# Optimization experiments

Hardware: AMD Instinct MI355X
Metric: run time of the kernel (lower is better)

The kernel has to match this reference:

```python
import jax, jax.numpy as jnp
import numpy as np

CAPACITY_FACTOR = 1.2


def setup_inputs() -> dict:
    key = jax.random.key(0)
    k1, k2 = jax.random.split(key, 2)
    D, E = 1024, 64
    x = jax.random.normal(k1, (8, 4096, D), dtype=jnp.float32)
    # xavier-uniform-ish router weight, zero bias (as in __init__)
    limit = np.sqrt(6.0 / (D + E)).astype(np.float32)
    W = jax.random.uniform(k2, (E, D), dtype=jnp.float32, minval=-limit, maxval=limit)
    b = jnp.zeros((E,), dtype=jnp.float32)
    return {"x": x, "W": W, "b": b, "detach_inputs": 0}


def reference(x, W, b, detach_inputs):
    bsz, seqlen, D = x.shape
    E = W.shape[0]                      # num experts == max_steps
    N = bsz * seqlen                    # num tokens
    x_flat = x.reshape(N, D)
    if detach_inputs:
        x_flat = jax.lax.stop_gradient(x_flat)
    logits = x_flat @ W.T + b           # [N, E]

    # expert-choice capacity (static python ints)
    k = max(1, int(N / max(1, E) * CAPACITY_FACTOR))
    k = min(k, N)

    # per-expert top-k over tokens: [E, k]
    topk_vals, topk_idx = jax.lax.top_k(logits.T, k)
    cand_tok = topk_idx.reshape(-1)                       # [E*k] token ids
    cand_exp = jnp.repeat(jnp.arange(E, dtype=jnp.int32), k)  # [E*k]
    cand_val = topk_vals.reshape(-1)                      # [E*k]

    # scatter-amax: best candidate logit per token (torch scatter_reduce_ 'amax')
    best_val = jnp.full((N,), -jnp.inf, dtype=logits.dtype).at[cand_tok].max(cand_val)

    # candidates that achieve the per-token max; dedup -> one expert per token
    # (tie-break: smallest expert index, matching first-occurrence after sort)
    eq = cand_val == best_val[cand_tok]
    exp_cand = jnp.where(eq, cand_exp, E).astype(jnp.int32)
    token_exp = jnp.full((N,), E, dtype=jnp.int32).at[cand_tok].min(exp_cand)
    selected = token_exp < E                              # token was picked by some expert
    assigned_expert = jnp.where(selected, token_exp, -1)  # [N], -1 = unassigned

    # load-balance loss from per-expert counts (bincount of assigned experts)
    sel_f = selected.astype(logits.dtype)
    counts = jnp.zeros((E,), dtype=logits.dtype).at[jnp.where(selected, token_exp, 0)].add(sel_f)
    mean_load = counts.mean()
    load_balance_loss = ((counts - mean_load) ** 2).mean() / (mean_load + 1e-9)

    best_val_out = jnp.where(selected, best_val, jnp.zeros((), logits.dtype))
    return (best_val_out, assigned_expert, selected, load_balance_loss)
```

## Files before the change

kernel.cpp:

```cpp
#include <hip/hip_runtime.h>
#include <math.h>

typedef __attribute__((ext_vector_type(4))) double d4;

__device__ inline unsigned fkey(float f) {
  unsigned bits = __float_as_uint(f);
  return (bits & 0x80000000u) ? ~bits : (bits | 0x80000000u);
}

__global__ __launch_bounds__(512, 4) void logits_fused_kernel(
    const float* __restrict__ x, const float* __restrict__ W,
    const float* __restrict__ bias, float* __restrict__ logits,
    float* __restrict__ logitsT, int N, int D) {
  __shared__ __attribute__((aligned(16))) double xs64[64 * 66];
  __shared__ __attribute__((aligned(16))) double ws64[64 * 66];
  __shared__ unsigned s_fl;

  const int tid = threadIdx.x;
  const int tok0 = blockIdx.x * 64;
  const int l = tid & 63;
  const int l15 = l & 15;
  const int lk = l >> 4;

  double* pA = ws64;
  double* pB = ws64 + 64;
  if (tid < 64) {
    pA[l15 * 4 + lk] = (double)(l15 * 4 + lk + 1);
    pB[lk * 16 + l15] = (double)(l15 * 7 + lk * 3 + 2);
  }
  __syncthreads();
  if (tid < 64) {
    double a = pA[l15 * 4 + lk];
    double b = pB[lk * 16 + l15];
    d4 pacc = (d4)0.0;
    pacc = __builtin_amdgcn_mfma_f64_16x16x4f64(a, b, pacc, 0, 0, 0);
    unsigned res = 4;
    for (int m = 3; m >= 0; --m) {
      bool ok = true;
#pragma unroll
      for (int i = 0; i < 4; ++i) {
        int tr_ = (m < 2) ? ((m == 0) ? 4 * lk + i : lk + 4 * i) : l15;
        int tc_ = (m < 2) ? l15 : ((m == 2) ? 4 * lk + i : lk + 4 * i);
        double ref = 0.0;
#pragma unroll
        for (int kk = 0; kk < 4; ++kk) ref += pA[tr_ * 4 + kk] * pB[kk * 16 + tc_];
        ok = ok && (pacc[i] == ref);
      }
      if (__all(ok)) res = (unsigned)m;
    }
    if (l == 0) s_fl = res;
  }
  __syncthreads();
  const unsigned fl = s_fl;
  __syncthreads();

  if (fl < 4u) {
    const int w = tid >> 6;
    const int rb = (w & 3) * 16;
    const int cb = (w >> 2) * 32;

    d4 acc[2];
    acc[0] = (d4)0.0;
    acc[1] = (d4)0.0;

    const int r0 = tid >> 4;
    const int c40 = tid & 15;

    float4 rx0, rx1, rw0, rw1;
    rx0 = *(const float4*)(x + (size_t)(tok0 + r0) * D + c40 * 4);
    rx1 = *(const float4*)(x + (size_t)(tok0 + 32 + r0) * D + c40 * 4);
    rw0 = *(const float4*)(W + (size_t)r0 * D + c40 * 4);
    rw1 = *(const float4*)(W + (size_t)(32 + r0) * D + c40 * 4);

    const int nch = D >> 6;
    const int xa0 = (rb + l15) * 66 + lk;
    const int ba0 = (cb + l15) * 66 + lk;

    for (int c = 0; c < nch; ++c) {
      {
        double* d0 = xs64 + r0 * 66 + c40 * 4;
        *(double2*)(d0) = make_double2((double)rx0.x, (double)rx0.y);
        *(double2*)(d0 + 2) = make_double2((double)rx0.z, (double)rx0.w);
        double* d1 = xs64 + (32 + r0) * 66 + c40 * 4;
        *(double2*)(d1) = make_double2((double)rx1.x, (double)rx1.y);
        *(double2*)(d1 + 2) = make_double2((double)rx1.z, (double)rx1.w);
        double* e0 = ws64 + r0 * 66 + c40 * 4;
        *(double2*)(e0) = make_double2((double)rw0.x, (double)rw0.y);
        *(double2*)(e0 + 2) = make_double2((double)rw0.z, (double)rw0.w);
        double* e1 = ws64 + (32 + r0) * 66 + c40 * 4;
        *(double2*)(e1) = make_double2((double)rw1.x, (double)rw1.y);
        *(double2*)(e1 + 2) = make_double2((double)rw1.z, (double)rw1.w);
      }
      __syncthreads();
      if (c + 1 < nch) {
        int kc = (c + 1) << 6;
        rx0 = *(const float4*)(x + (size_t)(tok0 + r0) * D + kc + c40 * 4);
        rx1 = *(const float4*)(x + (size_t)(tok0 + 32 + r0) * D + kc + c40 * 4);
        rw0 = *(const float4*)(W + (size_t)r0 * D + kc + c40 * 4);
        rw1 = *(const float4*)(W + (size_t)(32 + r0) * D + kc + c40 * 4);
      }
#pragma unroll
      for (int s = 0; s < 16; ++s) {
        double a = xs64[xa0 + 4 * s];
        double b0 = ws64[ba0 + 4 * s];
        double b1 = ws64[ba0 + 16 * 66 + 4 * s];
        acc[0] = __builtin_amdgcn_mfma_f64_16x16x4f64(a, b0, acc[0], 0, 0, 0);
        acc[1] = __builtin_amdgcn_mfma_f64_16x16x4f64(a, b1, acc[1], 0, 0, 0);
      }
      __syncthreads();
    }

    float* ls = (float*)xs64;
#pragma unroll
    for (int ct = 0; ct < 2; ++ct) {
#pragma unroll
      for (int i = 0; i < 4; ++i) {
        int tr_, tc_;
        if (fl < 2u) { tc_ = l15; tr_ = (fl == 0u) ? 4 * lk + i : lk + 4 * i; }
        else         { tr_ = l15; tc_ = (fl == 2u) ? 4 * lk + i : lk + 4 * i; }
        int col = cb + ct * 16 + tc_;
        ls[(rb + tr_) * 68 + col] = (float)(acc[ct][i] + (double)bias[col]);
      }
    }
    __syncthreads();
#pragma unroll
    for (int it = 0; it < 2; ++it) {
      int slot = it * 512 + tid;
      int row = slot >> 4, c4 = slot & 15;
      float4 v = {ls[row * 68 + c4 * 4 + 0], ls[row * 68 + c4 * 4 + 1],
                  ls[row * 68 + c4 * 4 + 2], ls[row * 68 + c4 * 4 + 3]};
      *(float4*)(logits + (size_t)(tok0 + row) * 64 + c4 * 4) = v;
    }
#pragma unroll
    for (int it = 0; it < 2; ++it) {
      int slot = it * 512 + tid;
      int e = slot >> 4, t4 = slot & 15;
      float4 v = {ls[(t4 * 4 + 0) * 68 + e], ls[(t4 * 4 + 1) * 68 + e],
                  ls[(t4 * 4 + 2) * 68 + e], ls[(t4 * 4 + 3) * 68 + e]};
      *(float4*)(logitsT + (size_t)e * N + tok0 + t4 * 4) = v;
    }
  } else {
    for (int o = tid; o < 64 * 64; o += 512) {
      int row = o >> 6, col = o & 63;
      const float* xp = x + (size_t)(tok0 + row) * D;
      const float* wp = W + (size_t)col * D;
      double s = 0.0;
      for (int kk = 0; kk < D; ++kk)
        s = fma((double)xp[kk], (double)wp[kk], s);
      float v = (float)(s + (double)bias[col]);
      logits[(size_t)(tok0 + row) * 64 + col] = v;
      logitsT[(size_t)col * N + tok0 + row] = v;
    }
  }
}

template <int KPT4>
__global__ __launch_bounds__(1024) void select_kernel(
    const float* __restrict__ logitsT, unsigned* __restrict__ ukeys,
    int N, int k) {
  __shared__ unsigned long long part[16];
  __shared__ unsigned s_cur;
  const int e = blockIdx.x;
  const int tid = threadIdx.x;
  const int wid = tid >> 6;
  const int lane = tid & 63;

  const float4* src = (const float4*)(logitsT + (size_t)e * N);
  unsigned key[KPT4 > 0 ? KPT4 * 4 : 4];
  if (KPT4 > 0) {
#pragma unroll
    for (int i = 0; i < (KPT4 > 0 ? KPT4 : 1); ++i) {
      float4 v = src[tid + i * 1024];
      key[i * 4 + 0] = fkey(v.x);
      key[i * 4 + 1] = fkey(v.y);
      key[i * 4 + 2] = fkey(v.z);
      key[i * 4 + 3] = fkey(v.w);
    }
  }

  unsigned cur = 0;
  for (int s = 30; s >= 0; s -= 2) {
    unsigned c1 = cur | (1u << s);
    unsigned c2 = cur | (2u << s);
    unsigned c3 = cur | (3u << s);
    unsigned n1 = 0, n2 = 0, n3 = 0;
    if (KPT4 > 0) {
#pragma unroll
      for (int i = 0; i < (KPT4 > 0 ? KPT4 * 4 : 1); ++i) {
        unsigned u = key[i];
        n1 += (u >= c1) ? 1u : 0u;
        n2 += (u >= c2) ? 1u : 0u;
        n3 += (u >= c3) ? 1u : 0u;
      }
    } else {
      for (int i = tid; i < (N >> 2); i += 1024) {
        float4 v = src[i];
        unsigned u0 = fkey(v.x), u1 = fkey(v.y), u2 = fkey(v.z), u3 = fkey(v.w);
        n1 += (u0 >= c1) + (u1 >= c1) + (u2 >= c1) + (u3 >= c1);
        n2 += (u0 >= c2) + (u1 >= c2) + (u2 >= c2) + (u3 >= c2);
        n3 += (u0 >= c3) + (u1 >= c3) + (u2 >= c3) + (u3 >= c3);
      }
    }
    unsigned long long pk = (unsigned long long)n1 |
                            ((unsigned long long)n2 << 21) |
                            ((unsigned long long)n3 << 42);
#pragma unroll
    for (int off = 32; off; off >>= 1) pk += __shfl_xor(pk, off);
    if (lane == 0) part[wid] = pk;
    __syncthreads();
    if (tid == 0) {
      unsigned long long t = 0;
#pragma unroll
      for (int w = 0; w < 16; ++w) t += part[w];
      unsigned m1 = (unsigned)(t & 0x1FFFFFu);
      unsigned m2 = (unsigned)((t >> 21) & 0x1FFFFFu);
      unsigned m3 = (unsigned)(t >> 42);
      unsigned kk = (unsigned)k;
      unsigned nxt = cur;
      if (m3 >= kk) nxt = c3;
      else if (m2 >= kk) nxt = c2;
      else if (m1 >= kk) nxt = c1;
      s_cur = nxt;
    }
    __syncthreads();
    cur = s_cur;
  }
  if (tid == 0) ukeys[e] = cur;
}

__global__ __launch_bounds__(256) void assign_kernel(
    const float* __restrict__ logits, const unsigned* __restrict__ ukeys,
    float* __restrict__ out, int N) {
  const int lane = threadIdx.x & 63;
  const int token = blockIdx.x * 4 + (threadIdx.x >> 6);

  float v = logits[(size_t)token * 64 + lane];
  unsigned u = fkey(v);
  bool cand = (u >= ukeys[lane]);
  float cv = cand ? v : -INFINITY;
  float m = cv;
#pragma unroll
  for (int off = 32; off; off >>= 1) m = fmaxf(m, __shfl_xor(m, off));
  unsigned long long mask = __ballot(cand && (v == m));
  bool sel = (mask != 0ull);
  int minexp = sel ? (__ffsll((long long)mask) - 1) : -1;

  if (lane == 0) {
    out[token] = sel ? m : 0.0f;
    out[N + token] = (float)minexp;
    out[2 * N + token] = sel ? 1.0f : 0.0f;
  }
}

__global__ __launch_bounds__(1024) void count_loss_kernel(
    const float* __restrict__ assigned, float* __restrict__ out, int N) {
  __shared__ unsigned hist[16][64];
  const int tid = threadIdx.x;
  const int wid = tid >> 6;
  hist[wid][tid & 63] = 0u;
  __syncthreads();
  const float4* src = (const float4*)assigned;
  for (int i = tid; i < (N >> 2); i += 1024) {
    float4 v = src[i];
    int e0 = (int)v.x, e1 = (int)v.y, e2 = (int)v.z, e3 = (int)v.w;
    if (e0 >= 0) atomicAdd(&hist[wid][e0], 1u);
    if (e1 >= 0) atomicAdd(&hist[wid][e1], 1u);
    if (e2 >= 0) atomicAdd(&hist[wid][e2], 1u);
    if (e3 >= 0) atomicAdd(&hist[wid][e3], 1u);
  }
  __syncthreads();
  if (tid < 64) {
    unsigned c = 0;
#pragma unroll
    for (int w = 0; w < 16; ++w) c += hist[w][tid];
    double cd = (double)c;
    double s = cd;
#pragma unroll
    for (int off = 32; off; off >>= 1) s += __shfl_xor(s, off);
    double mean = s / 64.0;
    double d = cd - mean;
    d = d * d;
#pragma unroll
    for (int off = 32; off; off >>= 1) d += __shfl_xor(d, off);
    if (tid == 0) out[3 * (size_t)N] = (float)((d / 64.0) / (mean + 1e-9));
  }
}

extern "C" void kernel_launch(void* const* d_in, const int* in_sizes, int n_in,
                              void* d_out, int out_size, void* d_ws, size_t ws_size,
                              hipStream_t stream) {
  const float* x = (const float*)d_in[0];
  const float* W = (const float*)d_in[1];
  const float* b = (const float*)d_in[2];

  const int E = in_sizes[2];
  const int D = in_sizes[1] / E;
  const int N = in_sizes[0] / D;

  int k = (int)((double)N / (double)(E > 1 ? E : 1) * 1.2);
  if (k < 1) k = 1;
  if (k > N) k = N;

  const size_t NE = (size_t)N * E;
  float* out = (float*)d_out;

  float* logits = (float*)d_ws;
  float* logitsT = logits + NE;
  unsigned* ukeys = (unsigned*)(logitsT + NE);

  logits_fused_kernel<<<N / 64, 512, 0, stream>>>(x, W, b, logits, logitsT,
                                                  N, D);
  if (N == 32768)
    select_kernel<8><<<64, 1024, 0, stream>>>(logitsT, ukeys, N, k);
  else
    select_kernel<0><<<64, 1024, 0, stream>>>(logitsT, ukeys, N, k);
  assign_kernel<<<N / 4, 256, 0, stream>>>(logits, ukeys, out, N);
  count_loss_kernel<<<1, 1024, 0, stream>>>(out + N, out, N);
}
```

Before: 131.0 us.

## Fuse assign and count-loss kernels; retile logits GEMM to 1024 threads

```diff
diff --git a/kernel.cpp b/kernel.cpp
--- a/kernel.cpp
+++ b/kernel.cpp
@@ -8,12 +8,13 @@
   return (bits & 0x80000000u) ? ~bits : (bits | 0x80000000u);
 }
 
-__global__ __launch_bounds__(512, 4) void logits_fused_kernel(
+__global__ __launch_bounds__(1024, 8) void logits_fused_kernel(
     const float* __restrict__ x, const float* __restrict__ W,
     const float* __restrict__ bias, float* __restrict__ logits,
-    float* __restrict__ logitsT, int N, int D) {
-  __shared__ __attribute__((aligned(16))) double xs64[64 * 66];
-  __shared__ __attribute__((aligned(16))) double ws64[64 * 66];
+    float* __restrict__ logitsT, unsigned* __restrict__ gz,
+    int N, int D) {
+  __shared__ __attribute__((aligned(16))) double xs64[64 * 34];
+  __shared__ __attribute__((aligned(16))) double ws64[64 * 34];
   __shared__ unsigned s_fl;
 
   const int tid = threadIdx.x;
@@ -21,6 +22,8 @@
   const int l = tid & 63;
   const int l15 = l & 15;
   const int lk = l >> 4;
+
+  if (blockIdx.x == 0 && tid < 65) gz[tid] = 0u;
 
   double* pA = ws64;
   double* pB = ws64 + 64;
@@ -57,90 +60,62 @@
   if (fl < 4u) {
     const int w = tid >> 6;
     const int rb = (w & 3) * 16;
-    const int cb = (w >> 2) * 32;
-
-    d4 acc[2];
-    acc[0] = (d4)0.0;
-    acc[1] = (d4)0.0;
-
-    const int r0 = tid >> 4;
-    const int c40 = tid & 15;
-
-    float4 rx0, rx1, rw0, rw1;
-    rx0 = *(const float4*)(x + (size_t)(tok0 + r0) * D + c40 * 4);
-    rx1 = *(const float4*)(x + (size_t)(tok0 + 32 + r0) * D + c40 * 4);
-    rw0 = *(const float4*)(W + (size_t)r0 * D + c40 * 4);
-    rw1 = *(const float4*)(W + (size_t)(32 + r0) * D + c40 * 4);
-
-    const int nch = D >> 6;
-    const int xa0 = (rb + l15) * 66 + lk;
-    const int ba0 = (cb + l15) * 66 + lk;
+    const int cb = (w >> 2) * 16;
+
+    d4 acc = (d4)0.0;
+
+    const int srow = (tid & 511) >> 3;
+    const int sc = tid & 7;
+    const bool isx = (tid < 512);
+    const float* gsrc = isx ? (x + (size_t)(tok0 + srow) * D + sc * 4)
+                            : (W + (size_t)srow * D + sc * 4);
+    double* ldst = (isx ? xs64 : ws64) + srow * 33 + sc * 4;
+
+    float4 rg = *(const float4*)gsrc;
+    const int nch = D >> 5;
+    const int xa0 = (rb + l15) * 33 + lk;
+    const int ba0 = (cb + l15) * 33 + lk;
 
     for (int c = 0; c < nch; ++c) {
-      {
-        double* d0 = xs64 + r0 * 66 + c40 * 4;
-        *(double2*)(d0) = make_double2((double)rx0.x, (double)rx0.y);
-        *(double2*)(d0 + 2) = make_double2((double)rx0.z, (double)rx0.w);
-        double* d1 = xs64 + (32 + r0) * 66 + c40 * 4;
-        *(double2*)(d1) = make_double2((double)rx1.x, (double)rx1.y);
-        *(double2*)(d1 + 2) = make_double2((double)rx1.z, (double)rx1.w);
-        double* e0 = ws64 + r0 * 66 + c40 * 4;
-        *(double2*)(e0) = make_double2((double)rw0.x, (double)rw0.y);
-        *(double2*)(e0 + 2) = make_double2((double)rw0.z, (double)rw0.w);
-        double* e1 = ws64 + (32 + r0) * 66 + c40 * 4;
-        *(double2*)(e1) = make_double2((double)rw1.x, (double)rw1.y);
-        *(double2*)(e1 + 2) = make_double2((double)rw1.z, (double)rw1.w);
+      ldst[0] = (double)rg.x;
+      ldst[1] = (double)rg.y;
+      ldst[2] = (double)rg.z;
+      ldst[3] = (double)rg.w;
+      __syncthreads();
+      if (c + 1 < nch) rg = *(const float4*)(gsrc + (c + 1) * 32);
+#pragma unroll
+      for (int s = 0; s < 8; ++s) {
+        double a = xs64[xa0 + 4 * s];
+        double b = ws64[ba0 + 4 * s];
+        acc = __builtin_amdgcn_mfma_f64_16x16x4f64(a, b, acc, 0, 0, 0);
       }
       __syncthreads();
-      if (c + 1 < nch) {
-        int kc = (c + 1) << 6;
-        rx0 = *(const float4*)(x + (size_t)(tok0 + r0) * D + kc + c40 * 4);
-        rx1 = *(const float4*)(x + (size_t)(tok0 + 32 + r0) * D + kc + c40 * 4);
-        rw0 = *(const float4*)(W + (size_t)r0 * D + kc + c40 * 4);
-        rw1 = *(const float4*)(W + (size_t)(32 + r0) * D + kc + c40 * 4);
-      }
-#pragma unroll
-      for (int s = 0; s < 16; ++s) {
-        double a = xs64[xa0 + 4 * s];
-        double b0 = ws64[ba0 + 4 * s];
-        double b1 = ws64[ba0 + 16 * 66 + 4 * s];
-        acc[0] = __builtin_amdgcn_mfma_f64_16x16x4f64(a, b0, acc[0], 0, 0, 0);
-        acc[1] = __builtin_amdgcn_mfma_f64_16x16x4f64(a, b1, acc[1], 0, 0, 0);
-      }
-      __syncthreads();
     }
 
     float* ls = (float*)xs64;
 #pragma unroll
-    for (int ct = 0; ct < 2; ++ct) {
-#pragma unroll
-      for (int i = 0; i < 4; ++i) {
-        int tr_, tc_;
-        if (fl < 2u) { tc_ = l15; tr_ = (fl == 0u) ? 4 * lk + i : lk + 4 * i; }
-        else         { tr_ = l15; tc_ = (fl == 2u) ? 4 * lk + i : lk + 4 * i; }
-        int col = cb + ct * 16 + tc_;
-        ls[(rb + tr_) * 68 + col] = (float)(acc[ct][i] + (double)bias[col]);
-      }
+    for (int i = 0; i < 4; ++i) {
+      int tr_, tc_;
+      if (fl < 2u) { tc_ = l15; tr_ = (fl == 0u) ? 4 * lk + i : lk + 4 * i; }
+      else         { tr_ = l15; tc_ = (fl == 2u) ? 4 * lk + i : lk + 4 * i; }
+      int col = cb + tc_;
+      ls[(rb + tr_) * 68 + col] = (float)(acc[i] + (double)bias[col]);
     }
     __syncthreads();
-#pragma unroll
-    for (int it = 0; it < 2; ++it) {
-      int slot = it * 512 + tid;
-      int row = slot >> 4, c4 = slot & 15;
+    {
+      int row = tid >> 4, c4 = tid & 15;
       float4 v = {ls[row * 68 + c4 * 4 + 0], ls[row * 68 + c4 * 4 + 1],
                   ls[row * 68 + c4 * 4 + 2], ls[row * 68 + c4 * 4 + 3]};
       *(float4*)(logits + (size_t)(tok0 + row) * 64 + c4 * 4) = v;
     }
-#pragma unroll
-    for (int it = 0; it < 2; ++it) {
-      int slot = it * 512 + tid;
-      int e = slot >> 4, t4 = slot & 15;
+    {
+      int e = tid >> 4, t4 = tid & 15;
       float4 v = {ls[(t4 * 4 + 0) * 68 + e], ls[(t4 * 4 + 1) * 68 + e],
                   ls[(t4 * 4 + 2) * 68 + e], ls[(t4 * 4 + 3) * 68 + e]};
       *(float4*)(logitsT + (size_t)e * N + tok0 + t4 * 4) = v;
     }
   } else {
-    for (int o = tid; o < 64 * 64; o += 512) {
+    for (int o = tid; o < 64 * 64; o += 1024) {
       int row = o >> 6, col = o & 63;
       const float* xp = x + (size_t)(tok0 + row) * D;
       const float* wp = W + (size_t)col * D;
@@ -228,61 +203,66 @@
   if (tid == 0) ukeys[e] = cur;
 }
 
-__global__ __launch_bounds__(256) void assign_kernel(
+__global__ __launch_bounds__(1024) void assign_count_kernel(
     const float* __restrict__ logits, const unsigned* __restrict__ ukeys,
-    float* __restrict__ out, int N) {
-  const int lane = threadIdx.x & 63;
-  const int token = blockIdx.x * 4 + (threadIdx.x >> 6);
-
-  float v = logits[(size_t)token * 64 + lane];
-  unsigned u = fkey(v);
-  bool cand = (u >= ukeys[lane]);
-  float cv = cand ? v : -INFINITY;
-  float m = cv;
-#pragma unroll
-  for (int off = 32; off; off >>= 1) m = fmaxf(m, __shfl_xor(m, off));
-  unsigned long long mask = __ballot(cand && (v == m));
-  bool sel = (mask != 0ull);
-  int minexp = sel ? (__ffsll((long long)mask) - 1) : -1;
-
-  if (lane == 0) {
-    out[token] = sel ? m : 0.0f;
-    out[N + token] = (float)minexp;
-    out[2 * N + token] = sel ? 1.0f : 0.0f;
-  }
-}
-
-__global__ __launch_bounds__(1024) void count_loss_kernel(
-    const float* __restrict__ assigned, float* __restrict__ out, int N) {
+    float* __restrict__ out, unsigned* __restrict__ gz, int N, int nblk) {
   __shared__ unsigned hist[16][64];
+  __shared__ unsigned s_last;
   const int tid = threadIdx.x;
   const int wid = tid >> 6;
-  hist[wid][tid & 63] = 0u;
-  __syncthreads();
-  const float4* src = (const float4*)assigned;
-  for (int i = tid; i < (N >> 2); i += 1024) {
-    float4 v = src[i];
-    int e0 = (int)v.x, e1 = (int)v.y, e2 = (int)v.z, e3 = (int)v.w;
-    if (e0 >= 0) atomicAdd(&hist[wid][e0], 1u);
-    if (e1 >= 0) atomicAdd(&hist[wid][e1], 1u);
-    if (e2 >= 0) atomicAdd(&hist[wid][e2], 1u);
-    if (e3 >= 0) atomicAdd(&hist[wid][e3], 1u);
+  const int lane = tid & 63;
+  hist[wid][lane] = 0u;
+  __syncthreads();
+
+  const unsigned uk = ukeys[lane];
+  const int wg = blockIdx.x * 16 + wid;
+  const int nw = nblk * 16;
+  for (int token = wg; token < N; token += nw) {
+    float v = logits[(size_t)token * 64 + lane];
+    unsigned u = fkey(v);
+    bool cand = (u >= uk);
+    float m = cand ? v : -INFINITY;
+#pragma unroll
+    for (int off = 32; off; off >>= 1) m = fmaxf(m, __shfl_xor(m, off));
+    unsigned long long mask = __ballot(cand && (v == m));
+    bool sel = (mask != 0ull);
+    int minexp = sel ? (__ffsll((long long)mask) - 1) : -1;
+    if (lane == 0) {
+      out[token] = sel ? m : 0.0f;
+      out[N + token] = (float)minexp;
+      out[2 * N + token] = sel ? 1.0f : 0.0f;
+      if (sel) hist[wid][minexp] += 1u;
+    }
   }
   __syncthreads();
   if (tid < 64) {
     unsigned c = 0;
 #pragma unroll
-    for (int w = 0; w < 16; ++w) c += hist[w][tid];
-    double cd = (double)c;
-    double s = cd;
-#pragma unroll
-    for (int off = 32; off; off >>= 1) s += __shfl_xor(s, off);
-    double mean = s / 64.0;
-    double d = cd - mean;
-    d = d * d;
-#pragma unroll
-    for (int off = 32; off; off >>= 1) d += __shfl_xor(d, off);
-    if (tid == 0) out[3 * (size_t)N] = (float)((d / 64.0) / (mean + 1e-9));
+    for (int w2 = 0; w2 < 16; ++w2) c += hist[w2][tid];
+    if (c) atomicAdd(&gz[tid], c);
+  }
+  __threadfence();
+  __syncthreads();
+  if (tid == 0) {
+    unsigned old = atomicAdd(&gz[64], 1u);
+    s_last = (old == (unsigned)(nblk - 1)) ? 1u : 0u;
+  }
+  __syncthreads();
+  if (s_last != 0u) {
+    __threadfence();
+    if (tid < 64) {
+      unsigned c = atomicAdd(&gz[tid], 0u);
+      double cd = (double)c;
+      double s = cd;
+#pragma unroll
+      for (int off = 32; off; off >>= 1) s += __shfl_xor(s, off);
+      double mean = s / 64.0;
+      double d = cd - mean;
+      d = d * d;
+#pragma unroll
+      for (int off = 32; off; off >>= 1) d += __shfl_xor(d, off);
+      if (tid == 0) out[3 * (size_t)N] = (float)((d / 64.0) / (mean + 1e-9));
+    }
   }
 }
 
@@ -307,13 +287,15 @@
   float* logits = (float*)d_ws;
   float* logitsT = logits + NE;
   unsigned* ukeys = (unsigned*)(logitsT + NE);
-
-  logits_fused_kernel<<<N / 64, 512, 0, stream>>>(x, W, b, logits, logitsT,
-                                                  N, D);
+  unsigned* gz = ukeys + 64;
+
+  logits_fused_kernel<<<N / 64, 1024, 0, stream>>>(x, W, b, logits, logitsT,
+                                                   gz, N, D);
   if (N == 32768)
     select_kernel<8><<<64, 1024, 0, stream>>>(logitsT, ukeys, N, k);
   else
     select_kernel<0><<<64, 1024, 0, stream>>>(logitsT, ukeys, N, k);
-  assign_kernel<<<N / 4, 256, 0, stream>>>(logits, ukeys, out, N);
-  count_loss_kernel<<<1, 1024, 0, stream>>>(out + N, out, N);
-}
+  const int nblk = 256;
+  assign_count_kernel<<<nblk, 1024, 0, stream>>>(logits, ukeys, out, gz, N,
+                                                 nblk);
+}
```

After: 187.3 us. 43.1% more time.
